# Kernel optimization log

Hardware: AMD Instinct MI355X
Metric: run time of the kernel (lower is better)

Reference implementation:

```python
import jax, jax.numpy as jnp
import numpy as np

H = 256  # hidden_representation_size

def setup_inputs() -> dict:
    key = jax.random.key(0)
    k1, k2 = jax.random.split(key)
    B, A, G, K = 32, 4096, 512, 16
    x = jax.random.normal(k1, (B, A * H), dtype=jnp.float32)
    idx = jax.random.randint(k2, (G, K), 0, A, dtype=jnp.int32)
    return {"x": x, "idx": idx}

def reference(x, idx):
    # x: [B, A*H]; idx: [G, K] action ids per related group (all groups non-empty)
    B = x.shape[0]
    xr = x.reshape(B, -1, H)            # [B, A, H]
    g = xr[:, idx, :]                    # gather -> [B, G, K, H]
    # original concatenates the K slices along the batch axis, then
    # GlobalMaxPooling1D maxes over that combined (B*K) axis -> [1, H] per group
    pooled = jnp.max(g, axis=(0, 2))     # [G, H]
    return pooled.reshape(1, -1)         # [1, G*H]
```

## Files before the change

### kernel.cpp

```cpp
#include <hip/hip_runtime.h>
#include <cfloat>

namespace {
constexpr int H = 256;
constexpr int A = 4096;
constexpr int B = 32;
constexpr int G = 512;
constexpr int K = 16;
constexpr size_t SLICE = (size_t)A * H;
}

static __device__ __forceinline__ float4 f4max(float4 a, float4 b) {
    float4 r;
    r.x = fmaxf(a.x, b.x);
    r.y = fmaxf(a.y, b.y);
    r.z = fmaxf(a.z, b.z);
    r.w = fmaxf(a.w, b.w);
    return r;
}

__global__ __launch_bounds__(256) void rowmax_kernel(const float* __restrict__ x,
                                                     float* __restrict__ rowmax) {
    const int t  = blockIdx.x * 256 + threadIdx.x;
    const size_t off = (size_t)t << 2;
    const float* p = x + off;

    float4 m0 = *(const float4*)p;
    float4 m1 = *(const float4*)(p + SLICE);
#pragma unroll
    for (int b = 2; b < B; b += 2) {
        float4 v0 = *(const float4*)(p + (size_t)b * SLICE);
        float4 v1 = *(const float4*)(p + (size_t)(b + 1) * SLICE);
        m0 = f4max(m0, v0);
        m1 = f4max(m1, v1);
    }
    *(float4*)(rowmax + off) = f4max(m0, m1);
}

__global__ __launch_bounds__(64) void gather_kernel(const float* __restrict__ rowmax,
                                                    const int* __restrict__ idx,
                                                    float* __restrict__ out) {
    const int g  = blockIdx.x;
    const int h4 = threadIdx.x << 2;

    float4 m = make_float4(-FLT_MAX, -FLT_MAX, -FLT_MAX, -FLT_MAX);
#pragma unroll
    for (int k = 0; k < K; ++k) {
        const int r = idx[g * K + k];
        float4 v = *(const float4*)(rowmax + (size_t)r * H + h4);
        m = f4max(m, v);
    }
    *(float4*)(out + (size_t)g * H + h4) = m;
}

__global__ __launch_bounds__(256) void fused_kernel(const float* __restrict__ x,
                                                    const int* __restrict__ idx,
                                                    float* __restrict__ out) {
    const int g    = blockIdx.x;
    const int lane = threadIdx.x & 63;
    const int wave = threadIdx.x >> 6;
    const int h4   = lane << 2;
    const int b0   = wave * 8;

    float4 m0 = make_float4(-FLT_MAX, -FLT_MAX, -FLT_MAX, -FLT_MAX);
    float4 m1 = m0;

    for (int k = 0; k < K; ++k) {
        const int r = idx[g * K + k];
        const float* p = x + (size_t)b0 * SLICE + (size_t)r * H + h4;
#pragma unroll
        for (int b = 0; b < 8; b += 2) {
            float4 v0 = *(const float4*)(p + (size_t)b * SLICE);
            float4 v1 = *(const float4*)(p + (size_t)(b + 1) * SLICE);
            m0 = f4max(m0, v0);
            m1 = f4max(m1, v1);
        }
    }
    float4 m = f4max(m0, m1);

    __shared__ float4 part[4][64];
    part[wave][lane] = m;
    __syncthreads();
    if (wave == 0) {
        float4 r = f4max(f4max(part[0][lane], part[1][lane]),
                         f4max(part[2][lane], part[3][lane]));
        *(float4*)(out + (size_t)g * H + h4) = r;
    }
}

extern "C" void kernel_launch(void* const* d_in, const int* in_sizes, int n_in,
                              void* d_out, int out_size, void* d_ws, size_t ws_size,
                              hipStream_t stream) {
    const float* x   = (const float*)d_in[0];
    const int*   idx = (const int*)d_in[1];
    float*       out = (float*)d_out;

    const size_t rowmax_bytes = (size_t)A * H * sizeof(float);
    if (ws_size >= rowmax_bytes) {
        float* rowmax = (float*)d_ws;
        rowmax_kernel<<<(A * H / 4) / 256, 256, 0, stream>>>(x, rowmax);
        gather_kernel<<<G, 64, 0, stream>>>(rowmax, idx, out);
    } else {
        fused_kernel<<<G, 256, 0, stream>>>(x, idx, out);
    }
}
```

Before: 194.6 us.

## Replace rowmax-plus-gather path with single fused gather-max kernel

Removes the two-kernel path, which reduced every action row across the batch into a workspace and then gathered from it. The launch now always uses the fused kernel, which reads only the rows named by idx for all batches and reduces them in one pass. The row indices are also loaded into registers up front. This drops a launch and the workspace round trip, but it issues more total gathered reads (duplicate rows across groups) from only 512 blocks, so it leans on cache hits and limited memory parallelism.

```diff
diff --git a/kernel.cpp b/kernel.cpp
--- a/kernel.cpp
+++ b/kernel.cpp
@@ -19,40 +19,6 @@
     return r;
 }
 
-__global__ __launch_bounds__(256) void rowmax_kernel(const float* __restrict__ x,
-                                                     float* __restrict__ rowmax) {
-    const int t  = blockIdx.x * 256 + threadIdx.x;
-    const size_t off = (size_t)t << 2;
-    const float* p = x + off;
-
-    float4 m0 = *(const float4*)p;
-    float4 m1 = *(const float4*)(p + SLICE);
-#pragma unroll
-    for (int b = 2; b < B; b += 2) {
-        float4 v0 = *(const float4*)(p + (size_t)b * SLICE);
-        float4 v1 = *(const float4*)(p + (size_t)(b + 1) * SLICE);
-        m0 = f4max(m0, v0);
-        m1 = f4max(m1, v1);
-    }
-    *(float4*)(rowmax + off) = f4max(m0, m1);
-}
-
-__global__ __launch_bounds__(64) void gather_kernel(const float* __restrict__ rowmax,
-                                                    const int* __restrict__ idx,
-                                                    float* __restrict__ out) {
-    const int g  = blockIdx.x;
-    const int h4 = threadIdx.x << 2;
-
-    float4 m = make_float4(-FLT_MAX, -FLT_MAX, -FLT_MAX, -FLT_MAX);
-#pragma unroll
-    for (int k = 0; k < K; ++k) {
-        const int r = idx[g * K + k];
-        float4 v = *(const float4*)(rowmax + (size_t)r * H + h4);
-        m = f4max(m, v);
-    }
-    *(float4*)(out + (size_t)g * H + h4) = m;
-}
-
 __global__ __launch_bounds__(256) void fused_kernel(const float* __restrict__ x,
                                                     const int* __restrict__ idx,
                                                     float* __restrict__ out) {
@@ -62,12 +28,15 @@
     const int h4   = lane << 2;
     const int b0   = wave * 8;
 
+    int rows[K];
+#pragma unroll
+    for (int k = 0; k < K; ++k) rows[k] = idx[g * K + k];
+
     float4 m0 = make_float4(-FLT_MAX, -FLT_MAX, -FLT_MAX, -FLT_MAX);
     float4 m1 = m0;
 
     for (int k = 0; k < K; ++k) {
-        const int r = idx[g * K + k];
-        const float* p = x + (size_t)b0 * SLICE + (size_t)r * H + h4;
+        const float* p = x + (size_t)b0 * SLICE + (size_t)rows[k] * H + h4;
 #pragma unroll
         for (int b = 0; b < 8; b += 2) {
             float4 v0 = *(const float4*)(p + (size_t)b * SLICE);
@@ -94,13 +63,7 @@
     const float* x   = (const float*)d_in[0];
     const int*   idx = (const int*)d_in[1];
     float*       out = (float*)d_out;
+    (void)d_ws; (void)ws_size;
 
-    const size_t rowmax_bytes = (size_t)A * H * sizeof(float);
-    if (ws_size >= rowmax_bytes) {
-        float* rowmax = (float*)d_ws;
-        rowmax_kernel<<<(A * H / 4) / 256, 256, 0, stream>>>(x, rowmax);
-        gather_kernel<<<G, 64, 0, stream>>>(rowmax, idx, out);
-    } else {
-        fused_kernel<<<G, 256, 0, stream>>>(x, idx, out);
-    }
+    fused_kernel<<<G, 256, 0, stream>>>(x, idx, out);
 }
```

Measured after the change: 198.2 us. About the same (+1.9%).
